# Optimization experiments

Hardware: AMD Instinct MI355X
Metric: run time of the kernel (lower is better)

The kernel has to match this reference:

```python
import jax, jax.numpy as jnp
import numpy as np

BLOCK_SIZE = 64
SPARSITY_RATIO = 0.5


def _band_mask(seq_len, block_size, sparsity_ratio):
    # Block (i, j) is computed iff max(0, i-w) <= j < min(nb, i+w), w = int(nb*ratio).
    nb = seq_len // block_size
    w = int(nb * sparsity_ratio)
    ib = jnp.arange(nb)
    bm = (ib[None, :] >= ib[:, None] - w) & (ib[None, :] < ib[:, None] + w)  # [nb, nb]
    return jnp.repeat(jnp.repeat(bm, block_size, axis=0), block_size, axis=1)  # [S, S]


def setup_inputs() -> dict:
    key = jax.random.key(0)
    kq, kk, kv = jax.random.split(key, 3)
    B, S, D = 4, 4096, 128
    return {
        "query": jax.random.normal(kq, (B, S, D), dtype=jnp.float32),
        "key": jax.random.normal(kk, (B, S, D), dtype=jnp.float32),
        "value": jax.random.normal(kv, (B, S, D), dtype=jnp.float32),
    }


def reference(query, key, value):
    B, S, D = query.shape
    mask = _band_mask(S, BLOCK_SIZE, SPARSITY_RATIO)  # [S, S] bool
    scores = jnp.einsum('bqd,bkd->bqk', query, key)  # [B, S, S]
    # Outside-band entries stay exactly 0 (NOT -inf) — matches torch.zeros init.
    scores = jnp.where(mask[None, :, :], scores, jnp.zeros((), scores.dtype))
    probs = jax.nn.softmax(scores, axis=-1)
    return jnp.matmul(probs, value)  # [B, S, D]
```

## Files before the change

### kernel.cpp

```cpp
#include <hip/hip_runtime.h>


typedef _Float16 f16;
typedef __attribute__((ext_vector_type(8))) _Float16 f16x8;
typedef __attribute__((ext_vector_type(4))) _Float16 f16x4;
typedef __attribute__((ext_vector_type(4))) float f32x4;

#define MFMA16(a, b, c) __builtin_amdgcn_mfma_f32_16x16x32_f16((a), (b), (c), 0, 0, 0)

#define BATCH 4
#define SEQ   4096
#define DIM   128
#define NB    64
#define WBAND 32
#define LOG2E 1.44269504088896f
#define DTHR  8.0f
#define TSTR  72

#define TILE  16384
#define CHUNKS 8
#define PART_STRIDE 16896

__device__ __forceinline__ void gl16(const char* g, char* l) {
  __builtin_amdgcn_global_load_lds(
      (const __attribute__((address_space(1))) void*)g,
      (__attribute__((address_space(3))) void*)l, 16, 0, 0);
}

__global__ __launch_bounds__(256) void convert_kernel(
    const float* __restrict__ K, const float* __restrict__ V,
    f16* __restrict__ KF, f16* __restrict__ VF, float* __restrict__ BS) {
  __shared__ f16 T[128 * TSTR];
  const int blk = blockIdx.x;
  const int b = blk >> 6, jb = blk & 63;
  const int s0 = jb * 64;
  const int t = threadIdx.x;

#pragma unroll
  for (int i = 0; i < 8; ++i) {
    int idx = t + i * 256;
    int row = idx >> 5;
    int c4 = (idx & 31) * 4;
    float4 v = *(const float4*)(V + (size_t)(b * SEQ + s0 + row) * DIM + c4);
    T[(c4 + 0) * TSTR + row] = (f16)v.x;
    T[(c4 + 1) * TSTR + row] = (f16)v.y;
    T[(c4 + 2) * TSTR + row] = (f16)v.z;
    T[(c4 + 3) * TSTR + row] = (f16)v.w;
  }

  char* kt = (char*)KF + (size_t)blk * TILE;
#pragma unroll
  for (int i = 0; i < 4; ++i) {
    int idx = t + i * 256;
    int frag = idx >> 6, lane = idx & 63;
    int ks = frag >> 2, jt = frag & 3;
    int row = jt * 16 + (lane & 15);
    int d0 = ks * 32 + (lane >> 4) * 8;
    const float* src = K + ((size_t)(b * SEQ + s0 + row)) * DIM + d0;
    float4 a = *(const float4*)src;
    float4 d = *(const float4*)(src + 4);
    f16x8 h = {(f16)a.x, (f16)a.y, (f16)a.z, (f16)a.w,
               (f16)d.x, (f16)d.y, (f16)d.z, (f16)d.w};
    *(f16x8*)(kt + idx * 16) = h;
  }
  __syncthreads();

  char* vt = (char*)VF + (size_t)blk * TILE;
#pragma unroll
  for (int i = 0; i < 4; ++i) {
    int idx = t + i * 256;
    int frag = idx >> 6, lane = idx & 63;
    int ks2 = frag >> 3, nt = frag & 7;
    int d = nt * 16 + (lane & 15);
    int k0 = ks2 * 32 + ((lane >> 4) & 3) * 4;
    f16x4 x = *(const f16x4*)(T + d * TSTR + k0);
    f16x4 y = *(const f16x4*)(T + d * TSTR + k0 + 16);
    f16x8 h = {x[0], x[1], x[2], x[3], y[0], y[1], y[2], y[3]};
    *(f16x8*)(vt + idx * 16) = h;
  }

  if (t < 128) {
    float s = 0.f;
    for (int k = 0; k < 64; ++k) s += (float)T[t * TSTR + k];
    BS[(b * NB + jb) * DIM + t] = s;
  }
}

__global__ __launch_bounds__(256, 2) void attn_kernel(
    const float* __restrict__ Q, const f16* __restrict__ KF,
    const f16* __restrict__ VF, char* __restrict__ PART) {
  __shared__ __align__(16) char smem[65536];

  const int id = blockIdx.x;
  const int lin = (id & 7) * 128 + (id >> 3);
  const int ck = lin & 7;
  const int pair = lin >> 3;
  const int b = pair >> 5, p = pair & 31;

  const int t = threadIdx.x;
  const int w = t >> 6, l = t & 63, lg = l >> 4, ll = l & 15;
  const int half = w >> 1, qh = w & 1;
  const int myib = p * 2 + half;

  const int jloU = max(0, p * 2 - WBAND);
  const int jhiU = min(NB, p * 2 + 1 + WBAND);
  const int lenU = jhiU - jloU;
  const int c = (lenU + CHUNKS - 1) >> 3;
  const int j0 = jloU + ck * c;
  const int nloc = min(c, jhiU - j0);
  const int mylo = max(0, myib - WBAND);
  const int myhi = min(NB, myib + WBAND);

  f16x8 qf[2][4];
#pragma unroll
  for (int s = 0; s < 2; ++s) {
    const float* qrow =
        Q + ((size_t)(b * SEQ + myib * 64 + qh * 32 + s * 16 + ll)) * DIM;
#pragma unroll
    for (int ks = 0; ks < 4; ++ks) {
      int d0 = ks * 32 + lg * 8;
      float4 a = *(const float4*)(qrow + d0);
      float4 cc = *(const float4*)(qrow + d0 + 4);
      float vv[8] = {a.x, a.y, a.z, a.w, cc.x, cc.y, cc.z, cc.w};
#pragma unroll
      for (int e = 0; e < 8; ++e) qf[s][ks][e] = (f16)(vv[e] * LOG2E);
    }
  }
  asm volatile("s_waitcnt vmcnt(0)" ::: "memory");

  float m2[2] = {0.f, 0.f};
  float ell[2] = {0.f, 0.f};
  f32x4 o[2][8];
#pragma unroll
  for (int s = 0; s < 2; ++s)
#pragma unroll
    for (int nt = 0; nt < 8; ++nt) o[s][nt] = (f32x4){0.f, 0.f, 0.f, 0.f};

  auto stage = [&](int buf, int jb) {
    const char* kg = (const char*)KF + ((size_t)(b * NB + jb)) * TILE + t * 16;
    const char* vg = (const char*)VF + ((size_t)(b * NB + jb)) * TILE + t * 16;
    char* kl = smem + buf * 32768 + t * 16;
#pragma unroll
    for (int i = 0; i < 4; ++i) gl16(kg + i * 4096, kl + i * 4096);
#pragma unroll
    for (int i = 0; i < 4; ++i) gl16(vg + i * 4096, kl + 16384 + i * 4096);
  };

  if (nloc > 0) {
    stage(0, j0);
    if (nloc > 1) stage(1, j0 + 1);

    for (int tt = 0; tt < nloc; ++tt) {
      if (tt + 1 < nloc) {
        asm volatile("s_waitcnt vmcnt(8)" ::: "memory");
      } else {
        asm volatile("s_waitcnt vmcnt(0)" ::: "memory");
      }
      __builtin_amdgcn_s_barrier();
      __builtin_amdgcn_sched_barrier(0);

      const int j = j0 + tt;
      const char* kb = smem + (tt & 1) * 32768;
      const char* vb = kb + 16384;

      if (j >= mylo && j < myhi) {
        f32x4 sacc[2][4];
#pragma unroll
        for (int s = 0; s < 2; ++s)
#pragma unroll
          for (int jt = 0; jt < 4; ++jt) sacc[s][jt] = (f32x4){0.f, 0.f, 0.f, 0.f};

        __builtin_amdgcn_s_setprio(1);
#pragma unroll
        for (int ks = 0; ks < 4; ++ks) {
#pragma unroll
          for (int jt = 0; jt < 4; ++jt) {
            f16x8 kf = *(const f16x8*)(kb + (ks * 4 + jt) * 1024 + l * 16);
            sacc[0][jt] = MFMA16(kf, qf[0][ks], sacc[0][jt]);
            sacc[1][jt] = MFMA16(kf, qf[1][ks], sacc[1][jt]);
          }
        }
        __builtin_amdgcn_s_setprio(0);

        f16x8 pa[2][2];
#pragma unroll
        for (int s = 0; s < 2; ++s) {
          float vm = sacc[s][0][0];
#pragma unroll
          for (int jt = 0; jt < 4; ++jt)
#pragma unroll
            for (int r = 0; r < 4; ++r) vm = fmaxf(vm, sacc[s][jt][r]);
          vm = fmaxf(vm, __shfl_xor(vm, 16));
          vm = fmaxf(vm, __shfl_xor(vm, 32));

          if (__any(vm - m2[s] > DTHR)) {
            float nm = fmaxf(m2[s], vm);
            float scl = __builtin_amdgcn_exp2f(m2[s] - nm);
            m2[s] = nm;
            ell[s] *= scl;
            float sb[4];
#pragma unroll
            for (int r = 0; r < 4; ++r) sb[r] = __shfl(scl, lg * 4 + r);
#pragma unroll
            for (int nt = 0; nt < 8; ++nt)
#pragma unroll
              for (int r = 0; r < 4; ++r) o[s][nt][r] *= sb[r];
          }

          float rsum = 0.f;
#pragma unroll
          for (int ks2 = 0; ks2 < 2; ++ks2) {
            f16x8 pv;
#pragma unroll
            for (int u = 0; u < 2; ++u) {
#pragma unroll
              for (int r = 0; r < 4; ++r) {
                float pe = __builtin_amdgcn_exp2f(sacc[s][ks2 * 2 + u][r] - m2[s]);
                rsum += pe;
                pv[u * 4 + r] = (f16)pe;
              }
            }
            pa[s][ks2] = pv;
          }
          ell[s] += rsum;
        }

        __builtin_amdgcn_s_setprio(1);
#pragma unroll
        for (int ks2 = 0; ks2 < 2; ++ks2) {
#pragma unroll
          for (int nt = 0; nt < 8; ++nt) {
            f16x8 vbf = *(const f16x8*)(vb + (ks2 * 8 + nt) * 1024 + l * 16);
            o[0][nt] = MFMA16(pa[0][ks2], vbf, o[0][nt]);
            o[1][nt] = MFMA16(pa[1][ks2], vbf, o[1][nt]);
          }
        }
        __builtin_amdgcn_s_setprio(0);
      }

      __builtin_amdgcn_s_barrier();
      if (tt + 2 < nloc) stage(tt & 1, j0 + tt + 2);
    }
  }

#pragma unroll
  for (int s = 0; s < 2; ++s) {
    ell[s] += __shfl_xor(ell[s], 16);
    ell[s] += __shfl_xor(ell[s], 32);
  }

  char* pb = PART + ((size_t)((pair * CHUNKS + ck) * 2 + half)) * PART_STRIDE;
#pragma unroll
  for (int s = 0; s < 2; ++s)
#pragma unroll
    for (int g = 0; g < 4; ++g) {
      f16x8 hh;
#pragma unroll
      for (int r = 0; r < 4; ++r) {
        hh[r] = (f16)o[s][2 * g][r];
        hh[4 + r] = (f16)o[s][2 * g + 1][r];
      }
      *(f16x8*)(pb + qh * 8192 + ((s * 4 + g) * 64 + l) * 16) = hh;
    }
  if (lg == 0) {
#pragma unroll
    for (int s = 0; s < 2; ++s)
      *(float2*)(pb + 16384 + (qh * 32 + s * 16 + ll) * 8) =
          make_float2(m2[s], ell[s]);
  }
}

__global__ __launch_bounds__(256) void merge_kernel(
    const char* __restrict__ PART, const float* __restrict__ BS,
    float* __restrict__ Out) {
  __shared__ float VoutS[DIM];
  __shared__ float mlS[CHUNKS][64][2];

  const int id = blockIdx.x;
  const int lin = (id & 7) * 32 + (id >> 3);
  const int pair = lin >> 1, half = lin & 1;
  const int b = pair >> 5;
  const int ib = (pair & 31) * 2 + half;
  const int t = threadIdx.x;
  const int l = t & 63, lg = (t >> 4) & 3, ll = t & 15;
  const int sub = (t >> 6) & 1, qh = t >> 7;

  const int jlo = max(0, ib - WBAND);
  const int jhi = min(NB, ib + WBAND);
  const float cnt_out = (float)(SEQ - (jhi - jlo) * 64);

  if (t < DIM) {
    float s = 0.f;
    for (int j = 0; j < jlo; ++j) s += BS[(b * NB + j) * DIM + t];
    for (int j = jhi; j < NB; ++j) s += BS[(b * NB + j) * DIM + t];
    VoutS[t] = s;
  }

  const size_t pb0 = ((size_t)(pair * CHUNKS * 2 + half)) * PART_STRIDE;
  for (int i = t; i < CHUNKS * 64; i += 256) {
    int k = i >> 6, row = i & 63;
    *(float2*)&mlS[k][row][0] = *(const float2*)(
        PART + pb0 + (size_t)k * 2 * PART_STRIDE + 16384 + row * 8);
  }
  __syncthreads();

  float aw[4][CHUNKS], en[4], inv[4];
#pragma unroll
  for (int r = 0; r < 4; ++r) {
    int row = qh * 32 + sub * 16 + lg * 4 + r;
    float M = mlS[0][row][0];
#pragma unroll
    for (int k = 1; k < CHUNKS; ++k) M = fmaxf(M, mlS[k][row][0]);
    en[r] = __builtin_amdgcn_exp2f(-M);
    float den = cnt_out * en[r];
#pragma unroll
    for (int k = 0; k < CHUNKS; ++k) {
      aw[r][k] = __builtin_amdgcn_exp2f(mlS[k][row][0] - M);
      den += aw[r][k] * mlS[k][row][1];
    }
    inv[r] = 1.f / den;
  }

  float acc[8][4];
#pragma unroll
  for (int nt = 0; nt < 8; ++nt)
#pragma unroll
    for (int r = 0; r < 4; ++r) acc[nt][r] = 0.f;

  for (int k = 0; k < CHUNKS; ++k) {
    const char* oc = PART + pb0 + (size_t)k * 2 * PART_STRIDE + qh * 8192;
#pragma unroll
    for (int g = 0; g < 4; ++g) {
      f16x8 h = *(const f16x8*)(oc + ((sub * 4 + g) * 64 + l) * 16);
#pragma unroll
      for (int r = 0; r < 4; ++r) {
        acc[2 * g][r] += aw[r][k] * (float)h[r];
        acc[2 * g + 1][r] += aw[r][k] * (float)h[4 + r];
      }
    }
  }

  const int q0 = ib * 64;
#pragma unroll
  for (int nt = 0; nt < 8; ++nt) {
    int col = nt * 16 + ll;
    float vout = VoutS[col];
#pragma unroll
    for (int r = 0; r < 4; ++r) {
      int row = qh * 32 + sub * 16 + lg * 4 + r;
      Out[((size_t)(b * SEQ + q0 + row)) * DIM + col] =
          (acc[nt][r] + en[r] * vout) * inv[r];
    }
  }
}

extern "C" void kernel_launch(void* const* d_in, const int* in_sizes, int n_in,
                              void* d_out, int out_size, void* d_ws, size_t ws_size,
                              hipStream_t stream) {
  const float* Q = (const float*)d_in[0];
  const float* K = (const float*)d_in[1];
  const float* V = (const float*)d_in[2];
  float* Out = (float*)d_out;

  char* ws = (char*)d_ws;
  f16* KF = (f16*)ws;
  f16* VF = (f16*)(ws + (size_t)BATCH * NB * TILE);
  float* BS = (float*)(ws + 2 * (size_t)BATCH * NB * TILE);
  char* PART = ws + 2 * (size_t)BATCH * NB * TILE + (size_t)BATCH * NB * DIM * 4;

  convert_kernel<<<dim3(BATCH * NB), 256, 0, stream>>>(K, V, KF, VF, BS);
  attn_kernel<<<dim3(BATCH * NB / 2 * CHUNKS), 256, 0, stream>>>(Q, KF, VF, PART);
  merge_kernel<<<dim3(BATCH * NB), 256, 0, stream>>>(PART, BS, Out);
}
```

Baseline: 66.22 us.

## Software-pipeline QK^T and PV across tiles with split K/V staging

```diff
diff --git a/kernel.cpp b/kernel.cpp
--- a/kernel.cpp
+++ b/kernel.cpp
@@ -14,12 +14,15 @@
 #define NB    64
 #define WBAND 32
 #define LOG2E 1.44269504088896f
-#define DTHR  8.0f
 #define TSTR  72
 
 #define TILE  16384
 #define CHUNKS 8
 #define PART_STRIDE 16896
+
+#define WAIT8 asm volatile("s_waitcnt vmcnt(8)" ::: "memory")
+#define WAIT4 asm volatile("s_waitcnt vmcnt(4)" ::: "memory")
+#define WAIT0 asm volatile("s_waitcnt vmcnt(0)" ::: "memory")
 
 __device__ __forceinline__ void gl16(const char* g, char* l) {
   __builtin_amdgcn_global_load_lds(
@@ -105,9 +108,9 @@
   const int jloU = max(0, p * 2 - WBAND);
   const int jhiU = min(NB, p * 2 + 1 + WBAND);
   const int lenU = jhiU - jloU;
-  const int c = (lenU + CHUNKS - 1) >> 3;
-  const int j0 = jloU + ck * c;
-  const int nloc = min(c, jhiU - j0);
+  const int base = lenU >> 3, rem = lenU & 7;
+  const int j0 = jloU + ck * base + min(ck, rem);
+  const int nloc = base + (ck < rem ? 1 : 0);
   const int mylo = max(0, myib - WBAND);
   const int myhi = min(NB, myib + WBAND);
 
@@ -126,7 +129,7 @@
       for (int e = 0; e < 8; ++e) qf[s][ks][e] = (f16)(vv[e] * LOG2E);
     }
   }
-  asm volatile("s_waitcnt vmcnt(0)" ::: "memory");
+  WAIT0;
 
   float m2[2] = {0.f, 0.f};
   float ell[2] = {0.f, 0.f};
@@ -136,111 +139,138 @@
 #pragma unroll
     for (int nt = 0; nt < 8; ++nt) o[s][nt] = (f32x4){0.f, 0.f, 0.f, 0.f};
 
-  auto stage = [&](int buf, int jb) {
+  auto stageK = [&](int buf, int jb) {
     const char* kg = (const char*)KF + ((size_t)(b * NB + jb)) * TILE + t * 16;
+    char* kl = smem + buf * 16384 + t * 16;
+#pragma unroll
+    for (int i = 0; i < 4; ++i) gl16(kg + i * 4096, kl + i * 4096);
+  };
+  auto stageV = [&](int buf, int jb) {
     const char* vg = (const char*)VF + ((size_t)(b * NB + jb)) * TILE + t * 16;
-    char* kl = smem + buf * 32768 + t * 16;
-#pragma unroll
-    for (int i = 0; i < 4; ++i) gl16(kg + i * 4096, kl + i * 4096);
-#pragma unroll
-    for (int i = 0; i < 4; ++i) gl16(vg + i * 4096, kl + 16384 + i * 4096);
+    char* vl = smem + 32768 + buf * 16384 + t * 16;
+#pragma unroll
+    for (int i = 0; i < 4; ++i) gl16(vg + i * 4096, vl + i * 4096);
   };
 
-  if (nloc > 0) {
-    stage(0, j0);
-    if (nloc > 1) stage(1, j0 + 1);
+  f16x8 paA[2][2];
+  bool have = false;
+
+  auto QKT = [&](f32x4 sacc[2][4], const char* kb) {
+    __builtin_amdgcn_s_setprio(1);
+#pragma unroll
+    for (int ks = 0; ks < 4; ++ks) {
+#pragma unroll
+      for (int jt = 0; jt < 4; ++jt) {
+        f16x8 kf = *(const f16x8*)(kb + (ks * 4 + jt) * 1024 + l * 16);
+        sacc[0][jt] = MFMA16(kf, qf[0][ks], sacc[0][jt]);
+        sacc[1][jt] = MFMA16(kf, qf[1][ks], sacc[1][jt]);
+      }
+    }
+    __builtin_amdgcn_s_setprio(0);
+  };
+  auto PV = [&](const char* vb) {
+    __builtin_amdgcn_s_setprio(1);
+#pragma unroll
+    for (int ks2 = 0; ks2 < 2; ++ks2) {
+#pragma unroll
+      for (int nt = 0; nt < 8; ++nt) {
+        f16x8 vbf = *(const f16x8*)(vb + (ks2 * 8 + nt) * 1024 + l * 16);
+        o[0][nt] = MFMA16(paA[0][ks2], vbf, o[0][nt]);
+        o[1][nt] = MFMA16(paA[1][ks2], vbf, o[1][nt]);
+      }
+    }
+    __builtin_amdgcn_s_setprio(0);
+  };
+  auto SOFTMAX = [&](const f32x4 sacc[2][4]) {
+#pragma unroll
+    for (int s = 0; s < 2; ++s) {
+      float vm = fmaxf(fmaxf(sacc[s][0][0], sacc[s][0][1]),
+                       fmaxf(sacc[s][0][2], sacc[s][0][3]));
+#pragma unroll
+      for (int jt = 1; jt < 4; ++jt)
+#pragma unroll
+        for (int r = 0; r < 4; ++r) vm = fmaxf(vm, sacc[s][jt][r]);
+      vm = fmaxf(vm, __shfl_xor(vm, 16));
+      vm = fmaxf(vm, __shfl_xor(vm, 32));
+      float nm = fmaxf(m2[s], vm);
+      float scl = __builtin_amdgcn_exp2f(m2[s] - nm);
+      m2[s] = nm;
+      float rsum = 0.f;
+#pragma unroll
+      for (int ks2 = 0; ks2 < 2; ++ks2) {
+        f16x8 pv;
+#pragma unroll
+        for (int u = 0; u < 2; ++u)
+#pragma unroll
+          for (int r = 0; r < 4; ++r) {
+            float pe = __builtin_amdgcn_exp2f(sacc[s][ks2 * 2 + u][r] - nm);
+            rsum += pe;
+            pv[u * 4 + r] = (f16)pe;
+          }
+        paA[s][ks2] = pv;
+      }
+      ell[s] = ell[s] * scl + rsum;
+      float sb[4];
+#pragma unroll
+      for (int r = 0; r < 4; ++r) sb[r] = __shfl(scl, lg * 4 + r);
+#pragma unroll
+      for (int nt = 0; nt < 8; ++nt)
+#pragma unroll
+        for (int r = 0; r < 4; ++r) o[s][nt][r] *= sb[r];
+    }
+  };
+
+  {
+    stageK(0, j0);
+    stageV(0, j0);
+    if (nloc > 1) stageK(1, j0 + 1);
 
     for (int tt = 0; tt < nloc; ++tt) {
-      if (tt + 1 < nloc) {
-        asm volatile("s_waitcnt vmcnt(8)" ::: "memory");
+      if (tt == 0) {
+        if (nloc > 1) { WAIT8; } else { WAIT4; }
+      } else if (tt + 1 < nloc) {
+        WAIT8;
       } else {
-        asm volatile("s_waitcnt vmcnt(0)" ::: "memory");
+        WAIT4;
       }
       __builtin_amdgcn_s_barrier();
       __builtin_amdgcn_sched_barrier(0);
 
       const int j = j0 + tt;
-      const char* kb = smem + (tt & 1) * 32768;
-      const char* vb = kb + 16384;
-
-      if (j >= mylo && j < myhi) {
+      const char* kb = smem + (tt & 1) * 16384;
+      const char* vb = smem + 32768 + ((tt - 1) & 1) * 16384;
+      const bool doQK = (j >= mylo) && (j < myhi);
+
+      if (doQK && have) {
         f32x4 sacc[2][4];
 #pragma unroll
         for (int s = 0; s < 2; ++s)
 #pragma unroll
           for (int jt = 0; jt < 4; ++jt) sacc[s][jt] = (f32x4){0.f, 0.f, 0.f, 0.f};
-
-        __builtin_amdgcn_s_setprio(1);
-#pragma unroll
-        for (int ks = 0; ks < 4; ++ks) {
-#pragma unroll
-          for (int jt = 0; jt < 4; ++jt) {
-            f16x8 kf = *(const f16x8*)(kb + (ks * 4 + jt) * 1024 + l * 16);
-            sacc[0][jt] = MFMA16(kf, qf[0][ks], sacc[0][jt]);
-            sacc[1][jt] = MFMA16(kf, qf[1][ks], sacc[1][jt]);
-          }
-        }
-        __builtin_amdgcn_s_setprio(0);
-
-        f16x8 pa[2][2];
-#pragma unroll
-        for (int s = 0; s < 2; ++s) {
-          float vm = sacc[s][0][0];
-#pragma unroll
-          for (int jt = 0; jt < 4; ++jt)
-#pragma unroll
-            for (int r = 0; r < 4; ++r) vm = fmaxf(vm, sacc[s][jt][r]);
-          vm = fmaxf(vm, __shfl_xor(vm, 16));
-          vm = fmaxf(vm, __shfl_xor(vm, 32));
-
-          if (__any(vm - m2[s] > DTHR)) {
-            float nm = fmaxf(m2[s], vm);
-            float scl = __builtin_amdgcn_exp2f(m2[s] - nm);
-            m2[s] = nm;
-            ell[s] *= scl;
-            float sb[4];
-#pragma unroll
-            for (int r = 0; r < 4; ++r) sb[r] = __shfl(scl, lg * 4 + r);
-#pragma unroll
-            for (int nt = 0; nt < 8; ++nt)
-#pragma unroll
-              for (int r = 0; r < 4; ++r) o[s][nt][r] *= sb[r];
-          }
-
-          float rsum = 0.f;
-#pragma unroll
-          for (int ks2 = 0; ks2 < 2; ++ks2) {
-            f16x8 pv;
-#pragma unroll
-            for (int u = 0; u < 2; ++u) {
-#pragma unroll
-              for (int r = 0; r < 4; ++r) {
-                float pe = __builtin_amdgcn_exp2f(sacc[s][ks2 * 2 + u][r] - m2[s]);
-                rsum += pe;
-                pv[u * 4 + r] = (f16)pe;
-              }
-            }
-            pa[s][ks2] = pv;
-          }
-          ell[s] += rsum;
-        }
-
-        __builtin_amdgcn_s_setprio(1);
-#pragma unroll
-        for (int ks2 = 0; ks2 < 2; ++ks2) {
-#pragma unroll
-          for (int nt = 0; nt < 8; ++nt) {
-            f16x8 vbf = *(const f16x8*)(vb + (ks2 * 8 + nt) * 1024 + l * 16);
-            o[0][nt] = MFMA16(pa[0][ks2], vbf, o[0][nt]);
-            o[1][nt] = MFMA16(pa[1][ks2], vbf, o[1][nt]);
-          }
-        }
-        __builtin_amdgcn_s_setprio(0);
-      }
+        QKT(sacc, kb);
+        PV(vb);
+        SOFTMAX(sacc);
+      } else if (doQK) {
+        f32x4 sacc[2][4];
+#pragma unroll
+        for (int s = 0; s < 2; ++s)
+#pragma unroll
+          for (int jt = 0; jt < 4; ++jt) sacc[s][jt] = (f32x4){0.f, 0.f, 0.f, 0.f};
+        QKT(sacc, kb);
+        SOFTMAX(sacc);
+      } else if (have) {
+        PV(vb);
+      }
+      have = doQK;
 
       __builtin_amdgcn_s_barrier();
-      if (tt + 2 < nloc) stage(tt & 1, j0 + tt + 2);
-    }
+      if (tt + 2 < nloc) stageK(tt & 1, j0 + tt + 2);
+      if (tt + 1 < nloc) stageV((tt + 1) & 1, j0 + tt + 1);
+    }
+
+    WAIT0;
+    __builtin_amdgcn_s_barrier();
+    if (have) PV(smem + 32768 + ((nloc - 1) & 1) * 16384);
   }
 
 #pragma unroll
```

Result: faster. 64.21 us (-3.0%).

## Load V directly to registers, single-buffer K in LDS, balance chunk split

Applied to the files above, without the earlier changes.

```diff
diff --git a/kernel.cpp b/kernel.cpp
--- a/kernel.cpp
+++ b/kernel.cpp
@@ -89,7 +89,7 @@
 __global__ __launch_bounds__(256, 2) void attn_kernel(
     const float* __restrict__ Q, const f16* __restrict__ KF,
     const f16* __restrict__ VF, char* __restrict__ PART) {
-  __shared__ __align__(16) char smem[65536];
+  __shared__ __align__(16) char smem[16384];
 
   const int id = blockIdx.x;
   const int lin = (id & 7) * 128 + (id >> 3);
@@ -105,9 +105,9 @@
   const int jloU = max(0, p * 2 - WBAND);
   const int jhiU = min(NB, p * 2 + 1 + WBAND);
   const int lenU = jhiU - jloU;
-  const int c = (lenU + CHUNKS - 1) >> 3;
-  const int j0 = jloU + ck * c;
-  const int nloc = min(c, jhiU - j0);
+  const int base = lenU >> 3, rem = lenU & 7;
+  const int j0 = jloU + ck * base + min(ck, rem);
+  const int nloc = base + (ck < rem ? 1 : 0);
   const int mylo = max(0, myib - WBAND);
   const int myhi = min(NB, myib + WBAND);
 
@@ -126,7 +126,6 @@
       for (int e = 0; e < 8; ++e) qf[s][ks][e] = (f16)(vv[e] * LOG2E);
     }
   }
-  asm volatile("s_waitcnt vmcnt(0)" ::: "memory");
 
   float m2[2] = {0.f, 0.f};
   float ell[2] = {0.f, 0.f};
@@ -136,111 +135,106 @@
 #pragma unroll
     for (int nt = 0; nt < 8; ++nt) o[s][nt] = (f32x4){0.f, 0.f, 0.f, 0.f};
 
-  auto stage = [&](int buf, int jb) {
+  auto stageK = [&](int jb) {
     const char* kg = (const char*)KF + ((size_t)(b * NB + jb)) * TILE + t * 16;
-    const char* vg = (const char*)VF + ((size_t)(b * NB + jb)) * TILE + t * 16;
-    char* kl = smem + buf * 32768 + t * 16;
-#pragma unroll
-    for (int i = 0; i < 4; ++i) gl16(kg + i * 4096, kl + i * 4096);
-#pragma unroll
-    for (int i = 0; i < 4; ++i) gl16(vg + i * 4096, kl + 16384 + i * 4096);
+#pragma unroll
+    for (int i = 0; i < 4; ++i) gl16(kg + i * 4096, smem + t * 16 + i * 4096);
   };
 
-  if (nloc > 0) {
-    stage(0, j0);
-    if (nloc > 1) stage(1, j0 + 1);
-
-    for (int tt = 0; tt < nloc; ++tt) {
-      if (tt + 1 < nloc) {
-        asm volatile("s_waitcnt vmcnt(8)" ::: "memory");
-      } else {
-        asm volatile("s_waitcnt vmcnt(0)" ::: "memory");
-      }
-      __builtin_amdgcn_s_barrier();
-      __builtin_amdgcn_sched_barrier(0);
-
-      const int j = j0 + tt;
-      const char* kb = smem + (tt & 1) * 32768;
-      const char* vb = kb + 16384;
-
-      if (j >= mylo && j < myhi) {
-        f32x4 sacc[2][4];
-#pragma unroll
-        for (int s = 0; s < 2; ++s)
-#pragma unroll
-          for (int jt = 0; jt < 4; ++jt) sacc[s][jt] = (f32x4){0.f, 0.f, 0.f, 0.f};
-
-        __builtin_amdgcn_s_setprio(1);
-#pragma unroll
-        for (int ks = 0; ks < 4; ++ks) {
-#pragma unroll
-          for (int jt = 0; jt < 4; ++jt) {
-            f16x8 kf = *(const f16x8*)(kb + (ks * 4 + jt) * 1024 + l * 16);
-            sacc[0][jt] = MFMA16(kf, qf[0][ks], sacc[0][jt]);
-            sacc[1][jt] = MFMA16(kf, qf[1][ks], sacc[1][jt]);
-          }
+  stageK(j0);
+  __syncthreads();
+
+  for (int tt = 0; tt < nloc; ++tt) {
+    const int j = j0 + tt;
+    if (j >= mylo && j < myhi) {
+      const char* vt =
+          (const char*)VF + ((size_t)(b * NB + j)) * TILE + (size_t)l * 16;
+      f16x8 vr0[8], vr1[8];
+#pragma unroll
+      for (int nt = 0; nt < 8; ++nt)
+        vr0[nt] = *(const f16x8*)(vt + nt * 1024);
+#pragma unroll
+      for (int nt = 0; nt < 8; ++nt)
+        vr1[nt] = *(const f16x8*)(vt + (8 + nt) * 1024);
+
+      f32x4 sacc[2][4];
+#pragma unroll
+      for (int s = 0; s < 2; ++s)
+#pragma unroll
+        for (int jt = 0; jt < 4; ++jt) sacc[s][jt] = (f32x4){0.f, 0.f, 0.f, 0.f};
+
+      __builtin_amdgcn_s_setprio(1);
+#pragma unroll
+      for (int ks = 0; ks < 4; ++ks) {
+#pragma unroll
+        for (int jt = 0; jt < 4; ++jt) {
+          f16x8 kf = *(const f16x8*)(smem + (ks * 4 + jt) * 1024 + l * 16);
+          sacc[0][jt] = MFMA16(kf, qf[0][ks], sacc[0][jt]);
+          sacc[1][jt] = MFMA16(kf, qf[1][ks], sacc[1][jt]);
         }
-        __builtin_amdgcn_s_setprio(0);
-
-        f16x8 pa[2][2];
-#pragma unroll
-        for (int s = 0; s < 2; ++s) {
-          float vm = sacc[s][0][0];
-#pragma unroll
-          for (int jt = 0; jt < 4; ++jt)
-#pragma unroll
-            for (int r = 0; r < 4; ++r) vm = fmaxf(vm, sacc[s][jt][r]);
-          vm = fmaxf(vm, __shfl_xor(vm, 16));
-          vm = fmaxf(vm, __shfl_xor(vm, 32));
-
-          if (__any(vm - m2[s] > DTHR)) {
-            float nm = fmaxf(m2[s], vm);
-            float scl = __builtin_amdgcn_exp2f(m2[s] - nm);
-            m2[s] = nm;
-            ell[s] *= scl;
-            float sb[4];
-#pragma unroll
-            for (int r = 0; r < 4; ++r) sb[r] = __shfl(scl, lg * 4 + r);
-#pragma unroll
-            for (int nt = 0; nt < 8; ++nt)
-#pragma unroll
-              for (int r = 0; r < 4; ++r) o[s][nt][r] *= sb[r];
-          }
-
-          float rsum = 0.f;
-#pragma unroll
-          for (int ks2 = 0; ks2 < 2; ++ks2) {
-            f16x8 pv;
-#pragma unroll
-            for (int u = 0; u < 2; ++u) {
-#pragma unroll
-              for (int r = 0; r < 4; ++r) {
-                float pe = __builtin_amdgcn_exp2f(sacc[s][ks2 * 2 + u][r] - m2[s]);
-                rsum += pe;
-                pv[u * 4 + r] = (f16)pe;
-              }
+      }
+      __builtin_amdgcn_s_setprio(0);
+
+      f16x8 pa[2][2];
+#pragma unroll
+      for (int s = 0; s < 2; ++s) {
+        float vm = fmaxf(fmaxf(sacc[s][0][0], sacc[s][0][1]),
+                         fmaxf(sacc[s][0][2], sacc[s][0][3]));
+#pragma unroll
+        for (int jt = 1; jt < 4; ++jt)
+#pragma unroll
+          for (int r = 0; r < 4; ++r) vm = fmaxf(vm, sacc[s][jt][r]);
+        vm = fmaxf(vm, __shfl_xor(vm, 16));
+        vm = fmaxf(vm, __shfl_xor(vm, 32));
+
+        if (__any(vm - m2[s] > DTHR)) {
+          float nm = fmaxf(m2[s], vm);
+          float scl = __builtin_amdgcn_exp2f(m2[s] - nm);
+          m2[s] = nm;
+          ell[s] *= scl;
+          float sb[4];
+#pragma unroll
+          for (int r = 0; r < 4; ++r) sb[r] = __shfl(scl, lg * 4 + r);
+#pragma unroll
+          for (int nt = 0; nt < 8; ++nt)
+#pragma unroll
+            for (int r = 0; r < 4; ++r) o[s][nt][r] *= sb[r];
+        }
+
+        float rsum = 0.f;
+#pragma unroll
+        for (int ks2 = 0; ks2 < 2; ++ks2) {
+          f16x8 pv;
+#pragma unroll
+          for (int u = 0; u < 2; ++u)
+#pragma unroll
+            for (int r = 0; r < 4; ++r) {
+              float pe = __builtin_amdgcn_exp2f(sacc[s][ks2 * 2 + u][r] - m2[s]);
+              rsum += pe;
+              pv[u * 4 + r] = (f16)pe;
             }
-            pa[s][ks2] = pv;
-          }
-          ell[s] += rsum;
+          pa[s][ks2] = pv;
         }
-
-        __builtin_amdgcn_s_setprio(1);
-#pragma unroll
-        for (int ks2 = 0; ks2 < 2; ++ks2) {
-#pragma unroll
-          for (int nt = 0; nt < 8; ++nt) {
-            f16x8 vbf = *(const f16x8*)(vb + (ks2 * 8 + nt) * 1024 + l * 16);
-            o[0][nt] = MFMA16(pa[0][ks2], vbf, o[0][nt]);
-            o[1][nt] = MFMA16(pa[1][ks2], vbf, o[1][nt]);
-          }
-        }
-        __builtin_amdgcn_s_setprio(0);
-      }
-
-      __builtin_amdgcn_s_barrier();
-      if (tt + 2 < nloc) stage(tt & 1, j0 + tt + 2);
-    }
+        ell[s] += rsum;
+      }
+
+      __builtin_amdgcn_s_setprio(1);
+#pragma unroll
+      for (int nt = 0; nt < 8; ++nt) {
+        o[0][nt] = MFMA16(pa[0][0], vr0[nt], o[0][nt]);
+        o[1][nt] = MFMA16(pa[1][0], vr0[nt], o[1][nt]);
+      }
+#pragma unroll
+      for (int nt = 0; nt < 8; ++nt) {
+        o[0][nt] = MFMA16(pa[0][1], vr1[nt], o[0][nt]);
+        o[1][nt] = MFMA16(pa[1][1], vr1[nt], o[1][nt]);
+      }
+      __builtin_amdgcn_s_setprio(0);
+    }
+
+    __syncthreads();
+    if (tt + 1 < nloc) stageK(j0 + tt + 1);
+    __syncthreads();
   }
 
 #pragma unroll
```

Measured after the change: 66.83 us. Within noise of the previous version (+0.9%).
